# Kernel tuning notes

Hardware: AMD Instinct MI355X
Metric: run time of the kernel (lower is better)

## Reference

```python
import jax, jax.numpy as jnp
import numpy as np

N = 50000      # nodes
E = 800000     # edges (avg degree 16)
IN_DIM = 128
H = 8          # num_heads
D = 16         # out_dim per head


def setup_inputs() -> dict:
    key = jax.random.key(0)
    ks = jax.random.split(key, 10)
    s = 1.0 / np.sqrt(IN_DIM)
    return {
        "h_src": jax.random.normal(ks[0], (N, IN_DIM), jnp.float32),
        "h_dst": jax.random.normal(ks[1], (N, IN_DIM), jnp.float32),
        "src": jax.random.randint(ks[2], (E,), 0, N),
        "dst": jax.random.randint(ks[3], (E,), 0, N),
        "Qw": jax.random.normal(ks[4], (IN_DIM, H * D), jnp.float32) * s,
        "Qb": jnp.zeros((H * D,), jnp.float32),
        "Kw": jax.random.normal(ks[5], (IN_DIM, H * D), jnp.float32) * s,
        "Kb": jnp.zeros((H * D,), jnp.float32),
        "Vw": jax.random.normal(ks[6], (IN_DIM, H * D), jnp.float32) * s,
        "Vb": jnp.zeros((H * D,), jnp.float32),
    }


def reference(h_src, h_dst, src, dst, Qw, Qb, Kw, Kb, Vw, Vb):
    # Node-level projections: [N, H, D]
    Q = (h_dst @ Qw + Qb).reshape(-1, H, D)
    K = (h_src @ Kw + Kb).reshape(-1, H, D)
    V = (h_src @ Vw + Vb).reshape(-1, H, D)
    # Edge-wise dot product per head: [E, H, 1]
    score = jnp.sum(K[src] * Q[dst], axis=-1, keepdims=True)
    # exp of clamped scaled score (note: clamp(-5,5) BEFORE exp, as in scaled_exp)
    score = jnp.exp(jnp.clip(score / jnp.float32(np.sqrt(D)), -5.0, 5.0))
    # Scatter-sum aggregation onto destination nodes
    wV = jax.ops.segment_sum(score * V[src], dst, num_segments=N)  # [N, H, D]
    z = jax.ops.segment_sum(score, dst, num_segments=N)            # [N, H, 1]
    return wV / z
```

## Files before the change

kernel.cpp:

```cpp
#include <hip/hip_runtime.h>
#include <hip/hip_bf16.h>
#include <math.h>

#define N_NODES 50000
#define E_EDGES 800000
#define IN_DIM  128
#define HD      128
#define SQRT_D_INV 0.25f

#define HIST_BLOCKS 512
#define PROJ_BLOCKS ((N_NODES + 63) / 64)

typedef __attribute__((ext_vector_type(8))) short short8v;
typedef __attribute__((ext_vector_type(4))) float float4v;

__device__ inline unsigned short f2bf(float x) {
    __hip_bfloat16 b = __float2bfloat16(x);
    return *reinterpret_cast<unsigned short*>(&b);
}
__device__ inline float bflo(unsigned int u) { return __uint_as_float(u << 16); }
__device__ inline float bfhi(unsigned int u) { return __uint_as_float(u & 0xffff0000u); }

__global__ __launch_bounds__(256) void wtr_init_kernel(
    const float* __restrict__ Qw, const float* __restrict__ Kw, const float* __restrict__ Vw,
    unsigned short* __restrict__ wt, int* __restrict__ counts8)
{
    int i = blockIdx.x * 256 + threadIdx.x;
    for (int j = i; j <= 8 * N_NODES; j += 392 * 256) counts8[j] = 0;
    if (i < 3 * 16384) {
        int which = i >> 14;
        int r = i & 16383;
        int k = r >> 7, n = r & 127;
        const float* W = (which == 0) ? Qw : (which == 1) ? Kw : Vw;
        wt[((size_t)which << 14) + n * 128 + k] = f2bf(W[r]);
    }
}

__global__ __launch_bounds__(512) void proj_hist_kernel(
    const float* __restrict__ h_src, const float* __restrict__ h_dst,
    const unsigned short* __restrict__ wt,
    const float* __restrict__ Qb, const float* __restrict__ Kb, const float* __restrict__ Vb,
    unsigned short* __restrict__ qkv,
    const int* __restrict__ dst, int* __restrict__ counts8, int* __restrict__ rank)
{
    if (blockIdx.x < HIST_BLOCKS) {
        const int hb = blockIdx.x;
        const int c = hb >> 6;
        int* cnt = counts8 + c * N_NODES;
        const int tid = hb * 512 + threadIdx.x;
        const int e3 = tid + 786432;
        const bool v3 = (e3 < E_EDGES);
        int d0 = dst[tid], d1 = dst[tid + 262144], d2 = dst[tid + 524288];
        int d3 = v3 ? dst[e3] : 0;
        int r0 = atomicAdd(&cnt[d0], 1);
        int r1 = atomicAdd(&cnt[d1], 1);
        int r2 = atomicAdd(&cnt[d2], 1);
        rank[tid] = r0; rank[tid + 262144] = r1; rank[tid + 524288] = r2;
        if (v3) rank[e3] = atomicAdd(&cnt[d3], 1);
        return;
    }

    __shared__ __align__(16) unsigned short smem[16384 + 8 * 1152];
    const int t  = threadIdx.x;
    const int w  = t >> 6;
    const int l  = t & 63;
    const int lr = l & 15;
    const int kg = l >> 4;
    const int wr = w & 3;
    const int wc = w >> 2;
    const int m_base = (blockIdx.x - HIST_BLOCKS) * 64 + wr * 16;
    const int arow = min(m_base + lr, N_NODES - 1);

    const float* pd = h_dst + (size_t)arow * IN_DIM;
    const float* ps = h_src + (size_t)arow * IN_DIM;

    short8v afd[4], afs[4];
    #pragma unroll
    for (int ks = 0; ks < 4; ++ks) {
        const int k0 = ks * 32 + kg * 8;
        float4 a0 = *(const float4*)&pd[k0];
        float4 a1 = *(const float4*)&pd[k0 + 4];
        float4 b0 = *(const float4*)&ps[k0];
        float4 b1 = *(const float4*)&ps[k0 + 4];
        afd[ks][0] = (short)f2bf(a0.x); afd[ks][1] = (short)f2bf(a0.y);
        afd[ks][2] = (short)f2bf(a0.z); afd[ks][3] = (short)f2bf(a0.w);
        afd[ks][4] = (short)f2bf(a1.x); afd[ks][5] = (short)f2bf(a1.y);
        afd[ks][6] = (short)f2bf(a1.z); afd[ks][7] = (short)f2bf(a1.w);
        afs[ks][0] = (short)f2bf(b0.x); afs[ks][1] = (short)f2bf(b0.y);
        afs[ks][2] = (short)f2bf(b0.z); afs[ks][3] = (short)f2bf(b0.w);
        afs[ks][4] = (short)f2bf(b1.x); afs[ks][5] = (short)f2bf(b1.y);
        afs[ks][6] = (short)f2bf(b1.z); afs[ks][7] = (short)f2bf(b1.w);
    }

    unsigned short* stg = &smem[16384 + w * 1152];

    #pragma unroll
    for (int phase = 0; phase < 3; ++phase) {
        const unsigned short* wsrc = wt + ((size_t)phase << 14);
        #pragma unroll
        for (int j = 0; j < 4; ++j) {
            const int selem = j * 4096 + t * 8;
            const int d = selem * 2;
            const int sd = d ^ (((d >> 8) & 7) << 4);
            *(short8v*)((char*)smem + sd) = *(const short8v*)&wsrc[selem];
        }
        __syncthreads();

        const short8v* aF = (phase == 0) ? afd : afs;
        float4v acc[4];
        #pragma unroll
        for (int i = 0; i < 4; ++i) acc[i] = (float4v)0.f;
        #pragma unroll
        for (int ks = 0; ks < 4; ++ks) {
            #pragma unroll
            for (int nf = 0; nf < 4; ++nf) {
                const int nfg = wc * 4 + nf;
                const int a = (nfg * 16 + lr) * 256 + ks * 64 + kg * 16;
                const int sa = a ^ ((lr & 7) << 4);
                short8v bf = *(const short8v*)((const char*)smem + sa);
                acc[nf] = __builtin_amdgcn_mfma_f32_16x16x32_bf16(aF[ks], bf, acc[nf], 0, 0, 0);
            }
        }

        const float* bias = (phase == 0) ? Qb : (phase == 1) ? Kb : Vb;
        #pragma unroll
        for (int nf = 0; nf < 4; ++nf) {
            const float b = bias[wc * 64 + nf * 16 + lr];
            #pragma unroll
            for (int r = 0; r < 4; ++r)
                stg[(kg * 4 + r) * 72 + nf * 16 + lr] = f2bf(acc[nf][r] + b);
        }
        #pragma unroll
        for (int i = 0; i < 2; ++i) {
            const int chunk = i * 64 + l;
            const int row = chunk >> 3;
            const int cc  = (chunk & 7) * 8;
            const int m = m_base + row;
            short8v v = *(const short8v*)&stg[row * 72 + cc];
            if (m < N_NODES)
                *(short8v*)&qkv[(size_t)m * 384 + phase * 128 + wc * 64 + cc] = v;
        }
        __syncthreads();
    }
}

__global__ __launch_bounds__(256) void offsets_kernel(const int* __restrict__ counts8,
                                                      int* __restrict__ begc,
                                                      int* __restrict__ begn,
                                                      int* __restrict__ cntn,
                                                      int* __restrict__ total) {
    int n = blockIdx.x * blockDim.x + threadIdx.x;
    int lane = threadIdx.x & 63;
    int pre[8];
    int s = 0;
    if (n < N_NODES) {
        #pragma unroll
        for (int c = 0; c < 8; ++c) {
            int v = counts8[c * N_NODES + n];
            pre[c] = s; s += v;
        }
    }
    int incl = s;
    #pragma unroll
    for (int off = 1; off < 64; off <<= 1) {
        int y = __shfl_up(incl, off);
        if (lane >= off) incl += y;
    }
    int wsum = __shfl(incl, 63);
    int base = 0;
    if (lane == 0) base = atomicAdd(total, wsum);
    base = __shfl(base, 0);
    int b = base + incl - s;
    if (n < N_NODES) {
        begn[n] = b; cntn[n] = s;
        #pragma unroll
        for (int c = 0; c < 8; ++c) begc[c * N_NODES + n] = b + pre[c];
    }
}

__global__ void scatter_kernel(const int* __restrict__ src, const int* __restrict__ dst,
                               const int* __restrict__ begc, const int* __restrict__ rank,
                               int* __restrict__ esrc) {
    int e = blockIdx.x * blockDim.x + threadIdx.x;
    if (e < E_EDGES) {
        int c = (e & 262143) >> 15;
        esrc[begc[c * N_NODES + dst[e]] + rank[e]] = src[e];
    }
}

__global__ __launch_bounds__(256) void agg_kernel(
    const unsigned short* __restrict__ qkv,
    const int* __restrict__ begp, const int* __restrict__ cntp,
    const int* __restrict__ esrc, float* __restrict__ out)
{
    int wave = (blockIdx.x * blockDim.x + threadIdx.x) >> 6;
    const int lane = threadIdx.x & 63;
    if (wave >= N_NODES) return;
    const int n = __builtin_amdgcn_readfirstlane(wave);
    const int e = lane >> 4;
    const int u = lane & 15;

    const uint4 qv = *(const uint4*)&qkv[(size_t)n * 384 + u * 8];
    const float q0 = bflo(qv.x), q1 = bfhi(qv.x), q2 = bflo(qv.y), q3 = bfhi(qv.y);
    const float q4 = bflo(qv.z), q5 = bfhi(qv.z), q6 = bflo(qv.w), q7 = bfhi(qv.w);

    const int b0 = begp[n], c0 = cntp[n], endp = b0 + c0;

    float a0=0.f,a1=0.f,a2=0.f,a3=0.f,a4=0.f,a5=0.f,a6=0.f,a7=0.f, z=0.f;

    for (int base = b0; base < endp; base += 16) {
        int idx[4];
        uint4 kk[4], vv[4];
        #pragma unroll
        for (int j = 0; j < 4; ++j) {
            idx[j] = base + j * 4 + e;
            const int s = esrc[min(idx[j], endp - 1)];
            const size_t ro = (size_t)s * 384;
            kk[j] = *(const uint4*)&qkv[ro + 128 + u * 8];
            vv[j] = *(const uint4*)&qkv[ro + 256 + u * 8];
        }
        #pragma unroll
        for (int j = 0; j < 4; ++j) {
            float d =      q0 * bflo(kk[j].x);
            d = fmaf(q1, bfhi(kk[j].x), d);
            d = fmaf(q2, bflo(kk[j].y), d);
            d = fmaf(q3, bfhi(kk[j].y), d);
            d = fmaf(q4, bflo(kk[j].z), d);
            d = fmaf(q5, bfhi(kk[j].z), d);
            d = fmaf(q6, bflo(kk[j].w), d);
            d = fmaf(q7, bfhi(kk[j].w), d);
            d += __shfl_xor(d, 1);
            float w = (idx[j] < endp) ? __expf(fminf(fmaxf(d * SQRT_D_INV, -5.f), 5.f)) : 0.f;
            z += w;
            a0 = fmaf(w, bflo(vv[j].x), a0);
            a1 = fmaf(w, bfhi(vv[j].x), a1);
            a2 = fmaf(w, bflo(vv[j].y), a2);
            a3 = fmaf(w, bfhi(vv[j].y), a3);
            a4 = fmaf(w, bflo(vv[j].z), a4);
            a5 = fmaf(w, bfhi(vv[j].z), a5);
            a6 = fmaf(w, bflo(vv[j].w), a6);
            a7 = fmaf(w, bfhi(vv[j].w), a7);
        }
    }

    #pragma unroll
    for (int mask = 16; mask <= 32; mask <<= 1) {
        z  += __shfl_xor(z, mask);
        a0 += __shfl_xor(a0, mask);
        a1 += __shfl_xor(a1, mask);
        a2 += __shfl_xor(a2, mask);
        a3 += __shfl_xor(a3, mask);
        a4 += __shfl_xor(a4, mask);
        a5 += __shfl_xor(a5, mask);
        a6 += __shfl_xor(a6, mask);
        a7 += __shfl_xor(a7, mask);
    }

    const float inv = 1.f / z;
    if (e == 0) {
        *(float4*)&out[(size_t)n * HD + u * 8]     = make_float4(a0*inv, a1*inv, a2*inv, a3*inv);
        *(float4*)&out[(size_t)n * HD + u * 8 + 4] = make_float4(a4*inv, a5*inv, a6*inv, a7*inv);
    }
}

extern "C" void kernel_launch(void* const* d_in, const int* in_sizes, int n_in,
                              void* d_out, int out_size, void* d_ws, size_t ws_size,
                              hipStream_t stream) {
    const float* h_src = (const float*)d_in[0];
    const float* h_dst = (const float*)d_in[1];
    const int*   src   = (const int*)d_in[2];
    const int*   dst   = (const int*)d_in[3];
    const float* Qw    = (const float*)d_in[4];
    const float* Qb    = (const float*)d_in[5];
    const float* Kw    = (const float*)d_in[6];
    const float* Kb    = (const float*)d_in[7];
    const float* Vw    = (const float*)d_in[8];
    const float* Vb    = (const float*)d_in[9];
    float* out = (float*)d_out;

    char* ws = (char*)d_ws;
    const size_t qkv_bytes = (size_t)N_NODES * 384 * sizeof(unsigned short);
    const size_t wt_bytes  = 3 * 128 * 128 * sizeof(unsigned short);
    unsigned short* qkvp = (unsigned short*)(ws);
    unsigned short* wtp  = (unsigned short*)(ws + qkv_bytes);
    int* counts8 = (int*)(ws + qkv_bytes + wt_bytes);
    int* total   = counts8 + 8 * N_NODES;
    int* begc    = counts8 + 8 * N_NODES + 1;
    int* begn    = begc + 8 * N_NODES;
    int* cntn    = begn + N_NODES;
    int* rank    = cntn + N_NODES;
    int* esrc    = rank + E_EDGES;

    wtr_init_kernel<<<392, 256, 0, stream>>>(Qw, Kw, Vw, wtp, counts8);

    proj_hist_kernel<<<HIST_BLOCKS + PROJ_BLOCKS, 512, 0, stream>>>(
        h_src, h_dst, wtp, Qb, Kb, Vb, qkvp, dst, counts8, rank);

    offsets_kernel<<<(N_NODES + 255) / 256, 256, 0, stream>>>(counts8, begc, begn, cntn, total);

    scatter_kernel<<<(E_EDGES + 255) / 256, 256, 0, stream>>>(src, dst, begc, rank, esrc);

    agg_kernel<<<(N_NODES * 64 + 255) / 256, 256, 0, stream>>>(qkvp, begn, cntn, esrc, out);
}
```

Before: 148.8 us.

## Split projection into independent per-wave 16-row tiles reading weights from global

Restructures the fused projection/histogram kernel: blocks shrink to 256 threads, and each wave now independently computes one 16-row by 64-column tile of Q, K or V. B fragments come straight from global/L2 instead of a block-wide LDS weight stage, and the per-block __syncthreads barriers are gone. This raises parallelism and removes barrier stalls and LDS weight staging, but each A row (h_dst/h_src) is now loaded and converted by more waves and the weights are fetched repeatedly from cache. The histogram part is remapped to 1024 blocks of 256 threads with the same 8-way counter split.

```diff
diff --git a/kernel.cpp b/kernel.cpp
--- a/kernel.cpp
+++ b/kernel.cpp
@@ -8,8 +8,10 @@
 #define HD      128
 #define SQRT_D_INV 0.25f
 
-#define HIST_BLOCKS 512
-#define PROJ_BLOCKS ((N_NODES + 63) / 64)
+#define HIST_BLOCKS 1024
+#define NT          3125
+#define PROJ_WAVES  (NT * 6)
+#define PROJ_BLOCKS ((PROJ_WAVES + 3) / 4)
 
 typedef __attribute__((ext_vector_type(8))) short short8v;
 typedef __attribute__((ext_vector_type(4))) float float4v;
@@ -36,7 +38,7 @@
     }
 }
 
-__global__ __launch_bounds__(512) void proj_hist_kernel(
+__global__ __launch_bounds__(256) void proj_hist_kernel(
     const float* __restrict__ h_src, const float* __restrict__ h_dst,
     const unsigned short* __restrict__ wt,
     const float* __restrict__ Qb, const float* __restrict__ Kb, const float* __restrict__ Vb,
@@ -45,9 +47,9 @@
 {
     if (blockIdx.x < HIST_BLOCKS) {
         const int hb = blockIdx.x;
-        const int c = hb >> 6;
+        const int c = hb >> 7;
         int* cnt = counts8 + c * N_NODES;
-        const int tid = hb * 512 + threadIdx.x;
+        const int tid = hb * 256 + threadIdx.x;
         const int e3 = tid + 786432;
         const bool v3 = (e3 < E_EDGES);
         int d0 = dst[tid], d1 = dst[tid + 262144], d2 = dst[tid + 524288];
@@ -60,87 +62,65 @@
         return;
     }
 
-    __shared__ __align__(16) unsigned short smem[16384 + 8 * 1152];
-    const int t  = threadIdx.x;
-    const int w  = t >> 6;
-    const int l  = t & 63;
+    __shared__ __align__(16) unsigned short smem[4][1152 + 8];
+    const int w  = threadIdx.x >> 6;
+    const int l  = threadIdx.x & 63;
+    const int gw = (blockIdx.x - HIST_BLOCKS) * 4 + w;
+    if (gw >= PROJ_WAVES) return;
+
+    const int rt    = gw / 6;
+    const int unit  = gw - rt * 6;
+    const int which = unit >> 1;
+    const int half  = unit & 1;
     const int lr = l & 15;
     const int kg = l >> 4;
-    const int wr = w & 3;
-    const int wc = w >> 2;
-    const int m_base = (blockIdx.x - HIST_BLOCKS) * 64 + wr * 16;
-    const int arow = min(m_base + lr, N_NODES - 1);
-
-    const float* pd = h_dst + (size_t)arow * IN_DIM;
-    const float* ps = h_src + (size_t)arow * IN_DIM;
-
-    short8v afd[4], afs[4];
+    const int m_base = rt * 16;
+
+    const float* A  = (which == 0) ? h_dst : h_src;
+    const float* ap = A + (size_t)(m_base + lr) * IN_DIM;
+
+    short8v af[4];
     #pragma unroll
     for (int ks = 0; ks < 4; ++ks) {
         const int k0 = ks * 32 + kg * 8;
-        float4 a0 = *(const float4*)&pd[k0];
-        float4 a1 = *(const float4*)&pd[k0 + 4];
-        float4 b0 = *(const float4*)&ps[k0];
-        float4 b1 = *(const float4*)&ps[k0 + 4];
-        afd[ks][0] = (short)f2bf(a0.x); afd[ks][1] = (short)f2bf(a0.y);
-        afd[ks][2] = (short)f2bf(a0.z); afd[ks][3] = (short)f2bf(a0.w);
-        afd[ks][4] = (short)f2bf(a1.x); afd[ks][5] = (short)f2bf(a1.y);
-        afd[ks][6] = (short)f2bf(a1.z); afd[ks][7] = (short)f2bf(a1.w);
-        afs[ks][0] = (short)f2bf(b0.x); afs[ks][1] = (short)f2bf(b0.y);
-        afs[ks][2] = (short)f2bf(b0.z); afs[ks][3] = (short)f2bf(b0.w);
-        afs[ks][4] = (short)f2bf(b1.x); afs[ks][5] = (short)f2bf(b1.y);
-        afs[ks][6] = (short)f2bf(b1.z); afs[ks][7] = (short)f2bf(b1.w);
-    }
-
-    unsigned short* stg = &smem[16384 + w * 1152];
-
-    #pragma unroll
-    for (int phase = 0; phase < 3; ++phase) {
-        const unsigned short* wsrc = wt + ((size_t)phase << 14);
-        #pragma unroll
-        for (int j = 0; j < 4; ++j) {
-            const int selem = j * 4096 + t * 8;
-            const int d = selem * 2;
-            const int sd = d ^ (((d >> 8) & 7) << 4);
-            *(short8v*)((char*)smem + sd) = *(const short8v*)&wsrc[selem];
-        }
-        __syncthreads();
-
-        const short8v* aF = (phase == 0) ? afd : afs;
-        float4v acc[4];
-        #pragma unroll
-        for (int i = 0; i < 4; ++i) acc[i] = (float4v)0.f;
-        #pragma unroll
-        for (int ks = 0; ks < 4; ++ks) {
-            #pragma unroll
-            for (int nf = 0; nf < 4; ++nf) {
-                const int nfg = wc * 4 + nf;
-                const int a = (nfg * 16 + lr) * 256 + ks * 64 + kg * 16;
-                const int sa = a ^ ((lr & 7) << 4);
-                short8v bf = *(const short8v*)((const char*)smem + sa);
-                acc[nf] = __builtin_amdgcn_mfma_f32_16x16x32_bf16(aF[ks], bf, acc[nf], 0, 0, 0);
-            }
-        }
-
-        const float* bias = (phase == 0) ? Qb : (phase == 1) ? Kb : Vb;
+        float4 a0 = *(const float4*)&ap[k0];
+        float4 a1 = *(const float4*)&ap[k0 + 4];
+        af[ks][0] = (short)f2bf(a0.x); af[ks][1] = (short)f2bf(a0.y);
+        af[ks][2] = (short)f2bf(a0.z); af[ks][3] = (short)f2bf(a0.w);
+        af[ks][4] = (short)f2bf(a1.x); af[ks][5] = (short)f2bf(a1.y);
+        af[ks][6] = (short)f2bf(a1.z); af[ks][7] = (short)f2bf(a1.w);
+    }
+
+    const unsigned short* W = wt + ((size_t)which << 14) + half * 64 * 128;
+    float4v acc[4];
+    #pragma unroll
+    for (int i = 0; i < 4; ++i) acc[i] = (float4v)0.f;
+    #pragma unroll
+    for (int ks = 0; ks < 4; ++ks) {
+        const int k0 = ks * 32 + kg * 8;
         #pragma unroll
         for (int nf = 0; nf < 4; ++nf) {
-            const float b = bias[wc * 64 + nf * 16 + lr];
-            #pragma unroll
-            for (int r = 0; r < 4; ++r)
-                stg[(kg * 4 + r) * 72 + nf * 16 + lr] = f2bf(acc[nf][r] + b);
-        }
-        #pragma unroll
-        for (int i = 0; i < 2; ++i) {
-            const int chunk = i * 64 + l;
-            const int row = chunk >> 3;
-            const int cc  = (chunk & 7) * 8;
-            const int m = m_base + row;
-            short8v v = *(const short8v*)&stg[row * 72 + cc];
-            if (m < N_NODES)
-                *(short8v*)&qkv[(size_t)m * 384 + phase * 128 + wc * 64 + cc] = v;
-        }
-        __syncthreads();
+            short8v bf = *(const short8v*)&W[(size_t)(nf * 16 + lr) * 128 + k0];
+            acc[nf] = __builtin_amdgcn_mfma_f32_16x16x32_bf16(af[ks], bf, acc[nf], 0, 0, 0);
+        }
+    }
+
+    const float* bias = (which == 0) ? Qb : (which == 1) ? Kb : Vb;
+    unsigned short* stg = &smem[w][0];
+    #pragma unroll
+    for (int nf = 0; nf < 4; ++nf) {
+        const float b = bias[half * 64 + nf * 16 + lr];
+        #pragma unroll
+        for (int r = 0; r < 4; ++r)
+            stg[(kg * 4 + r) * 72 + nf * 16 + lr] = f2bf(acc[nf][r] + b);
+    }
+    #pragma unroll
+    for (int i = 0; i < 2; ++i) {
+        const int chunk = i * 64 + l;
+        const int row = chunk >> 3;
+        const int cc  = (chunk & 7) * 8;
+        short8v v = *(const short8v*)&stg[row * 72 + cc];
+        *(short8v*)&qkv[(size_t)(m_base + row) * 384 + which * 128 + half * 64 + cc] = v;
     }
 }
 
@@ -293,7 +273,7 @@
 
     wtr_init_kernel<<<392, 256, 0, stream>>>(Qw, Kw, Vw, wtp, counts8);
 
-    proj_hist_kernel<<<HIST_BLOCKS + PROJ_BLOCKS, 512, 0, stream>>>(
+    proj_hist_kernel<<<HIST_BLOCKS + PROJ_BLOCKS, 256, 0, stream>>>(
         h_src, h_dst, wtp, Qb, Kb, Vb, qkvp, dst, counts8, rank);
 
     offsets_kernel<<<(N_NODES + 255) / 256, 256, 0, stream>>>(counts8, begc, begn, cntn, total);
```

Measured after the change: 174.8 us. 1.17x slower.
